# Performance work log

Measured on AMD Instinct MI355X. Metric: run time of the kernel, lower is better.

Reference implementation:

```python
import jax, jax.numpy as jnp
import numpy as np

B, T, E, H = 64, 320, 1024, 16
HS = E // H  # 64
EPS = 1e-5


def layernorm(x, w, b):
    mu = jnp.mean(x, axis=-1, keepdims=True)
    var = jnp.mean((x - mu) ** 2, axis=-1, keepdims=True)
    return (x - mu) * jax.lax.rsqrt(var + EPS) * w + b


def setup_inputs() -> dict:
    key = jax.random.key(0)
    ks = jax.random.split(key, 12)
    s_e = 1.0 / np.sqrt(E)
    s_f = 1.0 / np.sqrt(4 * E)
    return {
        "x": jax.random.normal(ks[0], (B, T, E), jnp.float32),
        "Wq": jax.random.uniform(ks[1], (H, E, HS), jnp.float32, -s_e, s_e),
        "Wk": jax.random.uniform(ks[2], (H, E, HS), jnp.float32, -s_e, s_e),
        "Wv": jax.random.uniform(ks[3], (H, E, HS), jnp.float32, -s_e, s_e),
        "Wo": jax.random.uniform(ks[4], (E, E), jnp.float32, -s_e, s_e),
        "bo": jax.random.uniform(ks[5], (E,), jnp.float32, -s_e, s_e),
        "W1": jax.random.uniform(ks[6], (E, 4 * E), jnp.float32, -s_e, s_e),
        "b1": jax.random.uniform(ks[7], (4 * E,), jnp.float32, -s_e, s_e),
        "W2": jax.random.uniform(ks[8], (4 * E, E), jnp.float32, -s_f, s_f),
        "b2": jax.random.uniform(ks[9], (E,), jnp.float32, -s_f, s_f),
        "ln1_w": jnp.ones((E,), jnp.float32),
        "ln1_b": jnp.zeros((E,), jnp.float32),
        "ln2_w": jnp.ones((E,), jnp.float32),
        "ln2_b": jnp.zeros((E,), jnp.float32),
    }


def reference(x, Wq, Wk, Wv, Wo, bo, W1, b1, W2, b2, ln1_w, ln1_b, ln2_w, ln2_b):
    # --- self-attention sublayer (dropout = identity in eval) ---
    h = layernorm(x, ln1_w, ln1_b)
    q = jnp.einsum("bte,hed->bhtd", h, Wq)
    k = jnp.einsum("bte,hed->bhtd", h, Wk)
    v = jnp.einsum("bte,hed->bhtd", h, Wv)
    # NOTE: original scales by full embedding dim C=E, not head_size
    scores = jnp.einsum("bhtd,bhsd->bhts", q, k) * (E ** -0.5)
    causal = jnp.tril(jnp.ones((T, T), bool))
    scores = jnp.where(causal, scores, -jnp.inf)
    wei = jax.nn.softmax(scores, axis=-1)
    attn = jnp.einsum("bhts,bhsd->bthd", wei, v).reshape(B, T, E)
    x = x + attn @ Wo + bo
    # --- feed-forward sublayer ---
    h2 = layernorm(x, ln2_w, ln2_b)
    x = x + jax.nn.relu(h2 @ W1 + b1) @ W2 + b2
    return x
```

## Files before the change

### kernel.cpp

```cpp
#include <hip/hip_runtime.h>


#define B_ 64
#define T_ 320
#define E_ 1024
#define H_ 16
#define HS_ 64
#define NTOK (B_ * T_)

typedef __attribute__((ext_vector_type(8))) __bf16 bf16x8;
typedef __attribute__((ext_vector_type(4))) float f32x4;

__device__ __forceinline__ unsigned short f2bf(float f) {
    unsigned u = __builtin_bit_cast(unsigned, f);
    u += 0x7fffu + ((u >> 16) & 1u);
    return (unsigned short)(u >> 16);
}
__device__ __forceinline__ float bf2f(unsigned short b) {
    return __builtin_bit_cast(float, (unsigned)b << 16);
}
__device__ __forceinline__ void gload16(const void* g, void* l) {
    __builtin_amdgcn_global_load_lds(
        (const __attribute__((address_space(1))) unsigned int*)g,
        (__attribute__((address_space(3))) unsigned int*)l, 16, 0, 0);
}

__global__ __launch_bounds__(256) void ln_kernel(const float* __restrict__ x,
                                                 const float* __restrict__ w,
                                                 const float* __restrict__ b,
                                                 unsigned short* __restrict__ y) {
    int row = blockIdx.x;
    int t = threadIdx.x;
    const float4* xr = (const float4*)(x + (size_t)row * E_);
    float4 v = xr[t];
    float s = v.x + v.y + v.z + v.w;
    float s2 = v.x * v.x + v.y * v.y + v.z * v.z + v.w * v.w;
#pragma unroll
    for (int o = 1; o < 64; o <<= 1) {
        s += __shfl_xor(s, o);
        s2 += __shfl_xor(s2, o);
    }
    __shared__ float rs[4], rs2[4];
    int wv = t >> 6;
    if ((t & 63) == 0) { rs[wv] = s; rs2[wv] = s2; }
    __syncthreads();
    s = rs[0] + rs[1] + rs[2] + rs[3];
    s2 = rs2[0] + rs2[1] + rs2[2] + rs2[3];
    float mu = s * (1.0f / E_);
    float var = s2 * (1.0f / E_) - mu * mu;
    float inv = rsqrtf(var + 1e-5f);
    float4 w4 = ((const float4*)w)[t];
    float4 b4 = ((const float4*)b)[t];
    ushort4 o4;
    o4.x = f2bf((v.x - mu) * inv * w4.x + b4.x);
    o4.y = f2bf((v.y - mu) * inv * w4.y + b4.y);
    o4.z = f2bf((v.z - mu) * inv * w4.z + b4.z);
    o4.w = f2bf((v.w - mu) * inv * w4.w + b4.w);
    *(ushort4*)(y + (size_t)row * E_ + 4 * t) = o4;
}

__global__ __launch_bounds__(256) void tcast_kernel(const float* __restrict__ src,
                                                    unsigned short* __restrict__ dst,
                                                    int K, int N, long sStride, long dStride) {
    src += (size_t)blockIdx.z * sStride;
    dst += (size_t)blockIdx.z * dStride;
    __shared__ float tile[64][65];
    int k0 = blockIdx.y * 64, n0 = blockIdx.x * 64;
    int tx = threadIdx.x & 63, ty = threadIdx.x >> 6;
#pragma unroll
    for (int r = ty; r < 64; r += 4)
        tile[r][tx] = src[(size_t)(k0 + r) * N + n0 + tx];
    __syncthreads();
#pragma unroll
    for (int r = ty; r < 64; r += 4)
        dst[(size_t)(n0 + r) * K + k0 + tx] = f2bf(tile[tx][r]);
}

template <bool BF16OUT, bool BIAS, bool RELU, bool RESID>
__global__ __launch_bounds__(256)
void gemm_mfma(const unsigned short* __restrict__ A,
               const unsigned short* __restrict__ Bt,
               const float* __restrict__ bias,
               const float* __restrict__ resid,
               void* __restrict__ Cout, int K, int N) {
    __shared__ uint4 A4[128 * 4];
    __shared__ uint4 B4[128 * 4];
    const int total = gridDim.x * gridDim.y;
    const int flat = blockIdx.y * gridDim.x + blockIdx.x;
    const int cpx = total >> 3;
    const int swz = (flat & 7) * cpx + (flat >> 3);
    const int m0 = (swz / gridDim.x) * 128;
    const int n0 = (swz % gridDim.x) * 128;

    const int tid = threadIdx.x;
    const int lane = tid & 63;
    const int wave = tid >> 6;
    const int wr = wave >> 1, wc = wave & 1;
    const int r16 = lane & 15;
    const int s = lane >> 4;
    const int sw = s ^ ((r16 >> 1) & 3);

    const int rin = lane >> 2;
    const int sl = lane & 3;
    const int gsl = sl ^ ((rin >> 1) & 3);
    const int rowA = wave * 32 + rin;
    const unsigned short* Ag0 = A + (size_t)(m0 + rowA) * K + gsl * 8;
    const unsigned short* Ag1 = Ag0 + (size_t)16 * K;
    const unsigned short* Bg0 = Bt + (size_t)(n0 + rowA) * K + gsl * 8;
    const unsigned short* Bg1 = Bg0 + (size_t)16 * K;
    uint4* ldsA0 = &A4[(wave * 32) * 4];
    uint4* ldsA1 = &A4[(wave * 32 + 16) * 4];
    uint4* ldsB0 = &B4[(wave * 32) * 4];
    uint4* ldsB1 = &B4[(wave * 32 + 16) * 4];

    f32x4 acc[4][4];
#pragma unroll
    for (int i = 0; i < 4; i++)
#pragma unroll
        for (int j = 0; j < 4; j++) acc[i][j] = (f32x4){0.f, 0.f, 0.f, 0.f};

    const bf16x8* Ab = (const bf16x8*)A4;
    const bf16x8* Bb = (const bf16x8*)B4;

    for (int k0 = 0; k0 < K; k0 += 32) {
        __syncthreads();
        gload16(Ag0 + k0, ldsA0);
        gload16(Ag1 + k0, ldsA1);
        gload16(Bg0 + k0, ldsB0);
        gload16(Bg1 + k0, ldsB1);
        __syncthreads();
        bf16x8 af[4], bf[4];
#pragma unroll
        for (int i = 0; i < 4; i++) {
            af[i] = Ab[(((wr << 6) + (i << 4) + r16) << 2) + sw];
            bf[i] = Bb[(((wc << 6) + (i << 4) + r16) << 2) + sw];
        }
#pragma unroll
        for (int i = 0; i < 4; i++)
#pragma unroll
            for (int j = 0; j < 4; j++)
                acc[i][j] = __builtin_amdgcn_mfma_f32_16x16x32_bf16(af[i], bf[j], acc[i][j], 0, 0, 0);
    }

    const int crow0 = m0 + wr * 64;
    const int ccol0 = n0 + wc * 64;
#pragma unroll
    for (int j = 0; j < 4; j++) {
        int gcol = ccol0 + j * 16 + r16;
        float bv = BIAS ? bias[gcol] : 0.f;
#pragma unroll
        for (int i = 0; i < 4; i++) {
            int growb = crow0 + i * 16 + s * 4;
#pragma unroll
            for (int r = 0; r < 4; r++) {
                float vo = acc[i][j][r] + bv;
                if (RELU) vo = fmaxf(vo, 0.f);
                int grow = growb + r;
                if (RESID) vo += resid[(size_t)grow * N + gcol];
                if (BF16OUT)
                    ((unsigned short*)Cout)[(size_t)grow * N + gcol] = f2bf(vo);
                else
                    ((float*)Cout)[(size_t)grow * N + gcol] = vo;
            }
        }
    }
}

__global__ __launch_bounds__(256) void attn_mfma(const unsigned short* __restrict__ qkv,
                                                 unsigned short* __restrict__ attn) {
    const int it = blockIdx.x;
    const int bh = blockIdx.y;
    const int b = bh >> 4, head = bh & 15;
    __shared__ uint4 KsV[512];
    __shared__ uint4 VtV[512];
    __shared__ uint4 PsV[4][128];
    unsigned short* Ks = (unsigned short*)KsV;
    unsigned short* Vt = (unsigned short*)VtV;

    const int tid = threadIdx.x;
    const int lane = tid & 63;
    const int w = tid >> 6;
    const int r16 = lane & 15;
    const int s = lane >> 4;
    unsigned short* P = (unsigned short*)PsV[w];

    const int qg = it * 64 + w * 16 + r16;
    const size_t qrow = (size_t)(b * T_ + qg) * 3072;

    bf16x8 qf0 = *(const bf16x8*)(qkv + qrow + head * 64 + 0 * 32 + s * 8);
    bf16x8 qf1 = *(const bf16x8*)(qkv + qrow + head * 64 + 1 * 32 + s * 8);

    f32x4 accO[4];
#pragma unroll
    for (int i = 0; i < 4; i++) accO[i] = (f32x4){0.f, 0.f, 0.f, 0.f};
    float m = -1e30f, l = 0.f;

    for (int j = 0; j <= it; j++) {
        __syncthreads();
#pragma unroll
        for (int half = 0; half < 2; half++) {
            int cid = tid + half * 256;
            int row = cid >> 3, sl = cid & 7;
            size_t tok = (size_t)(b * T_ + j * 64 + row) * 3072 + head * 64 + sl * 8;
            uint4 kc = *(const uint4*)(qkv + tok + 1024);
            uint4 vc = *(const uint4*)(qkv + tok + 2048);
            *(uint4*)(Ks + row * 64 + ((sl ^ (row & 7)) * 8)) = kc;
            union { uint4 u; unsigned short h[8]; } vv; vv.u = vc;
#pragma unroll
            for (int e = 0; e < 8; e++) {
                int d = sl * 8 + e;
                Vt[d * 64 + (((row >> 3) ^ (d & 7)) * 8) + (row & 7)] = vv.h[e];
            }
        }
        __syncthreads();

        f32x4 accS[4];
#pragma unroll
        for (int i = 0; i < 4; i++) accS[i] = (f32x4){0.f, 0.f, 0.f, 0.f};
#pragma unroll
        for (int c = 0; c < 2; c++) {
            bf16x8 qc = c ? qf1 : qf0;
#pragma unroll
            for (int i = 0; i < 4; i++) {
                int kvr = i * 16 + r16;
                bf16x8 kf = *(const bf16x8*)(Ks + kvr * 64 + (((c * 4 + s) ^ (kvr & 7)) * 8));
                accS[i] = __builtin_amdgcn_mfma_f32_16x16x32_bf16(kf, qc, accS[i], 0, 0, 0);
            }
        }

        float sv[16];
        float smax = -1e30f;
#pragma unroll
        for (int i = 0; i < 4; i++)
#pragma unroll
            for (int r = 0; r < 4; r++) {
                float vsc = accS[i][r] * 0.03125f;
                int kvg = j * 64 + i * 16 + 4 * s + r;
                if (kvg > qg) vsc = -1e30f;
                sv[i * 4 + r] = vsc;
                smax = fmaxf(smax, vsc);
            }
        smax = fmaxf(smax, __shfl_xor(smax, 16));
        smax = fmaxf(smax, __shfl_xor(smax, 32));
        float mn = fmaxf(m, smax);
        float al = __expf(m - mn);
        float ps = 0.f;
        unsigned short pb[16];
#pragma unroll
        for (int idx = 0; idx < 16; idx++) {
            float p = __expf(sv[idx] - mn);
            ps += p;
            pb[idx] = f2bf(p);
        }
        ps += __shfl_xor(ps, 16);
        ps += __shfl_xor(ps, 32);
        l = l * al + ps;
        m = mn;
#pragma unroll
        for (int i = 0; i < 4; i++)
#pragma unroll
            for (int r = 0; r < 4; r++) accO[i][r] *= al;

#pragma unroll
        for (int i = 0; i < 4; i++)
#pragma unroll
            for (int r = 0; r < 4; r++) {
                int kv = i * 16 + 4 * s + r;
                P[r16 * 64 + (((kv >> 3) ^ (r16 & 7)) * 8) + (kv & 7)] = pb[i * 4 + r];
            }
        asm volatile("s_waitcnt lgkmcnt(0)" ::: "memory");

#pragma unroll
        for (int c = 0; c < 2; c++) {
            bf16x8 pf = *(const bf16x8*)(P + r16 * 64 + (((c * 4 + s) ^ (r16 & 7)) * 8));
#pragma unroll
            for (int i = 0; i < 4; i++) {
                int d = i * 16 + r16;
                bf16x8 vf = *(const bf16x8*)(Vt + d * 64 + (((c * 4 + s) ^ (d & 7)) * 8));
                accO[i] = __builtin_amdgcn_mfma_f32_16x16x32_bf16(vf, pf, accO[i], 0, 0, 0);
            }
        }
    }

    float inv = 1.0f / l;
#pragma unroll
    for (int i = 0; i < 4; i++)
#pragma unroll
        for (int r = 0; r < 4; r++) {
            int d = i * 16 + 4 * s + r;
            P[r16 * 64 + (((d >> 3) ^ (r16 & 7)) * 8) + (d & 7)] = f2bf(accO[i][r] * inv);
        }
    asm volatile("s_waitcnt lgkmcnt(0)" ::: "memory");
#pragma unroll
    for (int half = 0; half < 2; half++) {
        int cid = lane + half * 64;
        int row = cid >> 3, sl = cid & 7;
        uint4 o = *(const uint4*)(P + row * 64 + ((sl ^ (row & 7)) * 8));
        *(uint4*)(attn + (size_t)(b * T_ + it * 64 + w * 16 + row) * E_ + head * 64 + sl * 8) = o;
    }
}

extern "C" void kernel_launch(void* const* d_in, const int* in_sizes, int n_in,
                              void* d_out, int out_size, void* d_ws, size_t ws_size,
                              hipStream_t stream) {
    const float* x    = (const float*)d_in[0];
    const float* Wq   = (const float*)d_in[1];
    const float* Wk   = (const float*)d_in[2];
    const float* Wv   = (const float*)d_in[3];
    const float* Wo   = (const float*)d_in[4];
    const float* bo   = (const float*)d_in[5];
    const float* W1   = (const float*)d_in[6];
    const float* b1   = (const float*)d_in[7];
    const float* W2   = (const float*)d_in[8];
    const float* b2   = (const float*)d_in[9];
    const float* ln1w = (const float*)d_in[10];
    const float* ln1b = (const float*)d_in[11];
    const float* ln2w = (const float*)d_in[12];
    const float* ln2b = (const float*)d_in[13];
    float* out = (float*)d_out;

    unsigned short* ws = (unsigned short*)d_ws;
    unsigned short* qkvWt = ws;
    unsigned short* WoT   = qkvWt + 3072 * 1024;
    unsigned short* W1T   = WoT + 1024 * 1024;
    unsigned short* W2T   = W1T + 4096 * 1024;
    unsigned short* hbuf  = W2T + 1024 * 4096;
    unsigned short* qkv   = hbuf + (size_t)NTOK * E_;
    unsigned short* abuf  = qkv + (size_t)NTOK * 3 * E_;
    unsigned short* inter = qkv;

    tcast_kernel<<<dim3(1, 16, 16), 256, 0, stream>>>(Wq, qkvWt, E_, HS_,
                                                      (long)E_ * HS_, (long)HS_ * E_);
    tcast_kernel<<<dim3(1, 16, 16), 256, 0, stream>>>(Wk, qkvWt + 1024 * 1024, E_, HS_,
                                                      (long)E_ * HS_, (long)HS_ * E_);
    tcast_kernel<<<dim3(1, 16, 16), 256, 0, stream>>>(Wv, qkvWt + 2048 * 1024, E_, HS_,
                                                      (long)E_ * HS_, (long)HS_ * E_);
    tcast_kernel<<<dim3(16, 16, 1), 256, 0, stream>>>(Wo, WoT, E_, E_, 0, 0);
    tcast_kernel<<<dim3(64, 16, 1), 256, 0, stream>>>(W1, W1T, E_, 4 * E_, 0, 0);
    tcast_kernel<<<dim3(16, 64, 1), 256, 0, stream>>>(W2, W2T, 4 * E_, E_, 0, 0);

    ln_kernel<<<NTOK, 256, 0, stream>>>(x, ln1w, ln1b, hbuf);
    gemm_mfma<true, false, false, false><<<dim3(24, 160), 256, 0, stream>>>(
        hbuf, qkvWt, nullptr, nullptr, qkv, 1024, 3072);
    attn_mfma<<<dim3(T_ / 64, B_ * H_), 256, 0, stream>>>(qkv, abuf);
    gemm_mfma<false, true, false, true><<<dim3(8, 160), 256, 0, stream>>>(
        abuf, WoT, bo, x, out, 1024, 1024);
    ln_kernel<<<NTOK, 256, 0, stream>>>(out, ln2w, ln2b, hbuf);
    gemm_mfma<true, true, true, false><<<dim3(32, 160), 256, 0, stream>>>(
        hbuf, W1T, b1, nullptr, inter, 1024, 4096);
    gemm_mfma<false, true, false, true><<<dim3(8, 160), 256, 0, stream>>>(
        inter, W2T, b2, out, out, 4096, 1024);
}
```

Baseline: 1.141 ms.

## Replace 128x128 GEMM with double-buffered 256x256 tile, 8-wave kernel

The GEMM kernel moves from 128x128 tiles with 4 waves to 256x256 tiles with 8 waves, each wave computing a 128x64 sub-tile split into two halves. LDS staging is double-buffered, so the next K-slice is loaded while MFMAs run on the current one, and s_setprio raises priority around the MFMA bursts. The aim is to increase operand reuse per byte loaded and to hide global-load latency. In exchange it uses more registers (launch bounds 512,2), more LDS, and fewer blocks per GEMM, which can worsen tail effects on the smaller N=1024 GEMMs.

```diff
diff --git a/kernel.cpp b/kernel.cpp
--- a/kernel.cpp
+++ b/kernel.cpp
@@ -77,82 +77,114 @@
 }
 
 template <bool BF16OUT, bool BIAS, bool RELU, bool RESID>
-__global__ __launch_bounds__(256)
-void gemm_mfma(const unsigned short* __restrict__ A,
-               const unsigned short* __restrict__ Bt,
-               const float* __restrict__ bias,
-               const float* __restrict__ resid,
-               void* __restrict__ Cout, int K, int N) {
-    __shared__ uint4 A4[128 * 4];
-    __shared__ uint4 B4[128 * 4];
+__global__ __launch_bounds__(512, 2)
+void gemm256(const unsigned short* __restrict__ A,
+             const unsigned short* __restrict__ Bt,
+             const float* __restrict__ bias,
+             const float* __restrict__ resid,
+             void* __restrict__ Cout, int K, int N) {
+    __shared__ unsigned short AS[2][256 * 32];
+    __shared__ unsigned short BS[2][256 * 32];
+
     const int total = gridDim.x * gridDim.y;
     const int flat = blockIdx.y * gridDim.x + blockIdx.x;
     const int cpx = total >> 3;
-    const int swz = (flat & 7) * cpx + (flat >> 3);
-    const int m0 = (swz / gridDim.x) * 128;
-    const int n0 = (swz % gridDim.x) * 128;
+    const int swzb = (flat & 7) * cpx + (flat >> 3);
+    const int m0 = (swzb / gridDim.x) << 8;
+    const int n0 = (swzb % gridDim.x) << 8;
 
     const int tid = threadIdx.x;
     const int lane = tid & 63;
     const int wave = tid >> 6;
-    const int wr = wave >> 1, wc = wave & 1;
+    const int wr = wave >> 2;
+    const int wc = wave & 3;
     const int r16 = lane & 15;
     const int s = lane >> 4;
     const int sw = s ^ ((r16 >> 1) & 3);
 
-    const int rin = lane >> 2;
-    const int sl = lane & 3;
-    const int gsl = sl ^ ((rin >> 1) & 3);
-    const int rowA = wave * 32 + rin;
-    const unsigned short* Ag0 = A + (size_t)(m0 + rowA) * K + gsl * 8;
-    const unsigned short* Ag1 = Ag0 + (size_t)16 * K;
-    const unsigned short* Bg0 = Bt + (size_t)(n0 + rowA) * K + gsl * 8;
-    const unsigned short* Bg1 = Bg0 + (size_t)16 * K;
-    uint4* ldsA0 = &A4[(wave * 32) * 4];
-    uint4* ldsA1 = &A4[(wave * 32 + 16) * 4];
-    uint4* ldsB0 = &B4[(wave * 32) * 4];
-    uint4* ldsB1 = &B4[(wave * 32 + 16) * 4];
-
-    f32x4 acc[4][4];
-#pragma unroll
-    for (int i = 0; i < 4; i++)
+    const int srow = tid >> 2;
+    const int ssl = tid & 3;
+    const int sgsl = ssl ^ (((srow & 15) >> 1) & 3);
+    const unsigned short* gA0 = A + (size_t)(m0 + srow) * K + sgsl * 8;
+    const unsigned short* gA1 = A + (size_t)(m0 + 128 + srow) * K + sgsl * 8;
+    const unsigned short* gB0 = Bt + (size_t)(n0 + srow) * K + sgsl * 8;
+    const unsigned short* gB1 = Bt + (size_t)(n0 + 128 + srow) * K + sgsl * 8;
+    const int wbase = wave * 512;
+
+    f32x4 acc[8][4];
+#pragma unroll
+    for (int i = 0; i < 8; i++)
 #pragma unroll
         for (int j = 0; j < 4; j++) acc[i][j] = (f32x4){0.f, 0.f, 0.f, 0.f};
 
-    const bf16x8* Ab = (const bf16x8*)A4;
-    const bf16x8* Bb = (const bf16x8*)B4;
-
-    for (int k0 = 0; k0 < K; k0 += 32) {
-        __syncthreads();
-        gload16(Ag0 + k0, ldsA0);
-        gload16(Ag1 + k0, ldsA1);
-        gload16(Bg0 + k0, ldsB0);
-        gload16(Bg1 + k0, ldsB1);
-        __syncthreads();
-        bf16x8 af[4], bf[4];
-#pragma unroll
-        for (int i = 0; i < 4; i++) {
-            af[i] = Ab[(((wr << 6) + (i << 4) + r16) << 2) + sw];
-            bf[i] = Bb[(((wc << 6) + (i << 4) + r16) << 2) + sw];
-        }
-#pragma unroll
-        for (int i = 0; i < 4; i++)
-#pragma unroll
-            for (int j = 0; j < 4; j++)
-                acc[i][j] = __builtin_amdgcn_mfma_f32_16x16x32_bf16(af[i], bf[j], acc[i][j], 0, 0, 0);
-    }
-
-    const int crow0 = m0 + wr * 64;
+    gload16(gA0, &AS[0][0 + wbase]);
+    gload16(gA1, &AS[0][4096 + wbase]);
+    gload16(gB0, &BS[0][0 + wbase]);
+    gload16(gB1, &BS[0][4096 + wbase]);
+    asm volatile("s_waitcnt vmcnt(0)" ::: "memory");
+    __builtin_amdgcn_s_barrier();
+
+    const int NT = K >> 5;
+    for (int t = 0; t < NT; ++t) {
+        const int cur = t & 1;
+        const int nxt = cur ^ 1;
+        const int k0n = (t + 1) << 5;
+        bf16x8 af[4], bfr[4];
+#pragma unroll
+        for (int f = 0; f < 4; ++f) {
+            int row = wr * 128 + f * 16 + r16;
+            af[f] = *(const bf16x8*)&AS[cur][row * 32 + sw * 8];
+        }
+#pragma unroll
+        for (int g = 0; g < 4; ++g) {
+            int row = wc * 64 + g * 16 + r16;
+            bfr[g] = *(const bf16x8*)&BS[cur][row * 32 + sw * 8];
+        }
+        if (t + 1 < NT) {
+            gload16(gA0 + k0n, &AS[nxt][0 + wbase]);
+            gload16(gA1 + k0n, &AS[nxt][4096 + wbase]);
+            gload16(gB0 + k0n, &BS[nxt][0 + wbase]);
+            gload16(gB1 + k0n, &BS[nxt][4096 + wbase]);
+        }
+        __builtin_amdgcn_s_barrier();
+        asm volatile("s_waitcnt lgkmcnt(0)" ::: "memory");
+        __builtin_amdgcn_s_setprio(1);
+#pragma unroll
+        for (int f = 0; f < 4; ++f)
+#pragma unroll
+            for (int g = 0; g < 4; ++g)
+                acc[f][g] = __builtin_amdgcn_mfma_f32_16x16x32_bf16(af[f], bfr[g], acc[f][g], 0, 0, 0);
+        __builtin_amdgcn_s_setprio(0);
+        __builtin_amdgcn_s_barrier();
+#pragma unroll
+        for (int f = 0; f < 4; ++f) {
+            int row = wr * 128 + 64 + f * 16 + r16;
+            af[f] = *(const bf16x8*)&AS[cur][row * 32 + sw * 8];
+        }
+        __builtin_amdgcn_s_barrier();
+        asm volatile("s_waitcnt lgkmcnt(0)" ::: "memory");
+        __builtin_amdgcn_s_setprio(1);
+#pragma unroll
+        for (int f = 0; f < 4; ++f)
+#pragma unroll
+            for (int g = 0; g < 4; ++g)
+                acc[4 + f][g] = __builtin_amdgcn_mfma_f32_16x16x32_bf16(af[f], bfr[g], acc[4 + f][g], 0, 0, 0);
+        __builtin_amdgcn_s_setprio(0);
+        asm volatile("s_waitcnt vmcnt(0)" ::: "memory");
+        __builtin_amdgcn_s_barrier();
+    }
+
+    const int crow0 = m0 + wr * 128;
     const int ccol0 = n0 + wc * 64;
 #pragma unroll
-    for (int j = 0; j < 4; j++) {
+    for (int j = 0; j < 4; ++j) {
         int gcol = ccol0 + j * 16 + r16;
         float bv = BIAS ? bias[gcol] : 0.f;
 #pragma unroll
-        for (int i = 0; i < 4; i++) {
+        for (int i = 0; i < 8; ++i) {
             int growb = crow0 + i * 16 + s * 4;
 #pragma unroll
-            for (int r = 0; r < 4; r++) {
+            for (int r = 0; r < 4; ++r) {
                 float vo = acc[i][j][r] + bv;
                 if (RELU) vo = fmaxf(vo, 0.f);
                 int grow = growb + r;
@@ -340,14 +372,14 @@
     tcast_kernel<<<dim3(16, 64, 1), 256, 0, stream>>>(W2, W2T, 4 * E_, E_, 0, 0);
 
     ln_kernel<<<NTOK, 256, 0, stream>>>(x, ln1w, ln1b, hbuf);
-    gemm_mfma<true, false, false, false><<<dim3(24, 160), 256, 0, stream>>>(
+    gemm256<true, false, false, false><<<dim3(12, 80), 512, 0, stream>>>(
         hbuf, qkvWt, nullptr, nullptr, qkv, 1024, 3072);
     attn_mfma<<<dim3(T_ / 64, B_ * H_), 256, 0, stream>>>(qkv, abuf);
-    gemm_mfma<false, true, false, true><<<dim3(8, 160), 256, 0, stream>>>(
+    gemm256<false, true, false, true><<<dim3(4, 80), 512, 0, stream>>>(
         abuf, WoT, bo, x, out, 1024, 1024);
     ln_kernel<<<NTOK, 256, 0, stream>>>(out, ln2w, ln2b, hbuf);
-    gemm_mfma<true, true, true, false><<<dim3(32, 160), 256, 0, stream>>>(
+    gemm256<true, true, true, false><<<dim3(16, 80), 512, 0, stream>>>(
         hbuf, W1T, b1, nullptr, inter, 1024, 4096);
-    gemm_mfma<false, true, false, true><<<dim3(8, 160), 256, 0, stream>>>(
+    gemm256<false, true, false, true><<<dim3(4, 80), 512, 0, stream>>>(
         inter, W2T, b2, out, out, 4096, 1024);
 }
```

Measured after the change: 1.248 ms. 9.4% more time.
